# Kernel optimization log

Measured on AMD Instinct MI355X. Metric: run time of the kernel, lower is better.

## Reference

```python
import jax, jax.numpy as jnp
import numpy as np

D_MODEL = 4096
EXPERTS = 64
TOPK = 2


def setup_inputs() -> dict:
    key = jax.random.key(0)
    kx, kw = jax.random.split(key)
    x = jax.random.normal(kx, (4, 4096, D_MODEL), dtype=jnp.float32)
    # nn.Linear(input_size, expert_num, bias=False) weight, stored as [D, E] for x @ W
    W = jax.random.normal(kw, (D_MODEL, EXPERTS), dtype=jnp.float32) * (1.0 / np.sqrt(D_MODEL))
    return {"x": x, "W": W}


def reference(x, W):
    # logits = GateL(x): [B, S, E]
    logits = jnp.einsum("bsd,de->bse", x, W)
    y = jax.nn.softmax(logits, axis=-1)
    # top-k mask: scatter ones at top-k expert slots, zero elsewhere
    _, topk_idx = jax.lax.top_k(y, TOPK)            # [B, S, k]
    mask = jnp.sum(jax.nn.one_hot(topk_idx, EXPERTS, dtype=y.dtype), axis=-2)  # [B, S, E]
    y = y * mask
    return (y, logits)
```

## Files before the change

### kernel.cpp

```cpp
#include <hip/hip_runtime.h>
#include <hip/hip_bf16.h>


typedef float f32x4 __attribute__((ext_vector_type(4)));
typedef __bf16 bf16x8 __attribute__((ext_vector_type(8)));

#define MFMA16(a, b, c) __builtin_amdgcn_mfma_f32_16x16x32_bf16((a), (b), (c), 0, 0, 0)

__global__ __launch_bounds__(256) void k_prep_w(const float* __restrict__ W,
                                                __bf16* __restrict__ wsW) {
  const int kc = blockIdx.x;
  const int t = threadIdx.x;
  const int kk0 = t >> 4;
  const int n0 = (t & 15) << 2;
  for (int i = 0; i < 2; ++i) {
    const int kk = kk0 + (i << 4);
    const float4 w4 = *(const float4*)(W + (size_t)(kc * 32 + kk) * 64 + n0);
    const float f[4] = {w4.x, w4.y, w4.z, w4.w};
    for (int j = 0; j < 4; ++j) {
      const int n = n0 + j;
      const __bf16 h = (__bf16)f[j];
      const __bf16 l = (__bf16)(f[j] - (float)h);
      const int base = (kc << 12) + ((n >> 4) << 10) + ((n & 15) << 5) + kk;
      wsW[base] = h;
      wsW[base + 512] = l;
    }
  }
}

__device__ __forceinline__ void split8(const float4 a, const float4 b,
                                       bf16x8& hi, bf16x8& lo) {
  const float f[8] = {a.x, a.y, a.z, a.w, b.x, b.y, b.z, b.w};
#pragma unroll
  for (int i = 0; i < 8; ++i) {
    const unsigned u = __builtin_bit_cast(unsigned, f[i]);
    hi[i] = __builtin_bit_cast(__bf16, (unsigned short)(u >> 16));
    lo[i] = (__bf16)(f[i] - __builtin_bit_cast(float, u & 0xFFFF0000u));
  }
}

__global__ __launch_bounds__(256, 2) void k_gate(const float* __restrict__ x,
                                                 const __bf16* __restrict__ wsW,
                                                 float* __restrict__ y,
                                                 float* __restrict__ logits) {
  const int t = threadIdx.x;
  const int w = t >> 6, l = t & 63;
  const int tb = blockIdx.x * 32;
  const int mt = w & 1, nh = w >> 1;
  const int q = l >> 4, ln = l & 15;

  const float* xp = x + (size_t)(tb + mt * 16 + ln) * 4096 + q * 8;
  const __bf16* wq = wsW + nh * 2048 + ln * 32 + q * 8;
  const __bf16* wp0 = wq;
  const __bf16* wp1 = wq + 4096;
  const __bf16* wp2 = wq + 8192;
  const __bf16* wp3 = wq + 12288;

  f32x4 acc0 = {0.f, 0.f, 0.f, 0.f};
  f32x4 acc1 = {0.f, 0.f, 0.f, 0.f};

  float4 xa[4], xb[4];
  bf16x8 wh0[4], wl0[4], wh1[4], wl1[4];

#define LOADX(S) do {                                                   \
    xa[S] = *(const float4*)(xp + (S) * 32);                            \
    xb[S] = *(const float4*)(xp + (S) * 32 + 4);                        \
  } while (0)
#define LOADW(S, P) do {                                                \
    wh0[S] = *(const bf16x8*)((P));                                     \
    wl0[S] = *(const bf16x8*)((P) + 512);                               \
    wh1[S] = *(const bf16x8*)((P) + 1024);                              \
    wl1[S] = *(const bf16x8*)((P) + 1536);                              \
  } while (0)
#define COMP(S) do {                                                    \
    bf16x8 ah, al;                                                      \
    split8(xa[S], xb[S], ah, al);                                       \
    acc0 = MFMA16(ah, wh0[S], acc0);                                    \
    acc0 = MFMA16(al, wh0[S], acc0);                                    \
    acc0 = MFMA16(ah, wl0[S], acc0);                                    \
    acc0 = MFMA16(al, wl0[S], acc0);                                    \
    acc1 = MFMA16(ah, wh1[S], acc1);                                    \
    acc1 = MFMA16(al, wh1[S], acc1);                                    \
    acc1 = MFMA16(ah, wl1[S], acc1);                                    \
    acc1 = MFMA16(al, wl1[S], acc1);                                    \
  } while (0)

  LOADX(0); LOADX(1); LOADX(2); LOADX(3);
  LOADW(0, wp0); LOADW(1, wp1); LOADW(2, wp2); LOADW(3, wp3);
  xp += 128; wp0 += 16384; wp1 += 16384; wp2 += 16384; wp3 += 16384;

  for (int it = 0; it < 31; ++it) {
    COMP(0); LOADX(0); LOADW(0, wp0);
    COMP(1); LOADX(1); LOADW(1, wp1);
    COMP(2); LOADX(2); LOADW(2, wp2);
    COMP(3); LOADX(3); LOADW(3, wp3);
    xp += 128; wp0 += 16384; wp1 += 16384; wp2 += 16384; wp3 += 16384;
  }
  COMP(0); COMP(1); COMP(2); COMP(3);
#undef LOADX
#undef LOADW
#undef COMP

  __shared__ float lt[32 * 65];
  const int col = nh * 32 + ln;
#pragma unroll
  for (int r = 0; r < 4; ++r) {
    const int row = mt * 16 + q * 4 + r;
    lt[row * 65 + col] = acc0[r];
    lt[row * 65 + col + 16] = acc1[r];
    logits[(size_t)(tb + row) * 64 + col] = acc0[r];
    logits[(size_t)(tb + row) * 64 + col + 16] = acc1[r];
  }
  __syncthreads();

#pragma unroll
  for (int i = 0; i < 8; ++i) {
    const int tok = w * 8 + i;
    const float v = lt[tok * 65 + l];
    float bv = v; int bi = l;
    for (int off = 32; off; off >>= 1) {
      const float ov = __shfl_xor(bv, off);
      const int oi = __shfl_xor(bi, off);
      if (ov > bv || (ov == bv && oi < bi)) { bv = ov; bi = oi; }
    }
    const int i1 = bi;
    const float m1 = bv;
    float cv = (l == i1) ? -3.402823466e38f : v;
    int ci = l;
    for (int off = 32; off; off >>= 1) {
      const float ov = __shfl_xor(cv, off);
      const int oi = __shfl_xor(ci, off);
      if (ov > cv || (ov == cv && oi < ci)) { cv = ov; ci = oi; }
    }
    const float e = __expf(v - m1);
    float s = e;
    for (int off = 32; off; off >>= 1) s += __shfl_xor(s, off);
    y[(size_t)(tb + tok) * 64 + l] = (l == i1 || l == ci) ? (e / s) : 0.0f;
  }
}

extern "C" void kernel_launch(void* const* d_in, const int* in_sizes, int n_in,
                              void* d_out, int out_size, void* d_ws, size_t ws_size,
                              hipStream_t stream) {
  (void)in_sizes; (void)n_in; (void)out_size; (void)ws_size;
  const float* x = (const float*)d_in[0];
  const float* W = (const float*)d_in[1];
  float* out = (float*)d_out;
  float* yout = out;
  float* logits = out + 1048576;
  __bf16* wsW = (__bf16*)d_ws;

  k_prep_w<<<128, 256, 0, stream>>>(W, wsW);
  k_gate<<<512, 256, 0, stream>>>(x, wsW, yout, logits);
}
```

Before: 404.5 us.

## Stream x and W tiles through LDS with async global_load_lds pipeline

```diff
diff --git a/kernel.cpp b/kernel.cpp
--- a/kernel.cpp
+++ b/kernel.cpp
@@ -7,28 +7,32 @@
 
 #define MFMA16(a, b, c) __builtin_amdgcn_mfma_f32_16x16x32_bf16((a), (b), (c), 0, 0, 0)
 
+__device__ __forceinline__ void gload_lds16(const void* g, void* l) {
+  __builtin_amdgcn_global_load_lds((const __attribute__((address_space(1))) void*)g,
+                                   (__attribute__((address_space(3))) void*)l, 16, 0, 0);
+}
+
 __global__ __launch_bounds__(256) void k_prep_w(const float* __restrict__ W,
                                                 __bf16* __restrict__ wsW) {
-  const int kc = blockIdx.x;
+  const int c = blockIdx.x;
   const int t = threadIdx.x;
-  const int kk0 = t >> 4;
-  const int n0 = (t & 15) << 2;
-  for (int i = 0; i < 2; ++i) {
-    const int kk = kk0 + (i << 4);
-    const float4 w4 = *(const float4*)(W + (size_t)(kc * 32 + kk) * 64 + n0);
-    const float f[4] = {w4.x, w4.y, w4.z, w4.w};
-    for (int j = 0; j < 4; ++j) {
-      const int n = n0 + j;
-      const __bf16 h = (__bf16)f[j];
-      const __bf16 l = (__bf16)(f[j] - (float)h);
-      const int base = (kc << 12) + ((n >> 4) << 10) + ((n & 15) << 5) + kk;
-      wsW[base] = h;
-      wsW[base + 512] = l;
-    }
+  const int e = t & 63;
+  const int q = t >> 6;
+  const int nh = e >> 5, ntl = (e >> 4) & 1, ln = e & 15;
+  bf16x8 hi8, lo8;
+#pragma unroll
+  for (int j = 0; j < 8; ++j) {
+    const float w = W[(size_t)(c * 32 + q * 8 + j) * 64 + e];
+    const __bf16 h = (__bf16)w;
+    hi8[j] = h;
+    lo8[j] = (__bf16)(w - (float)h);
   }
+  __bf16* base = wsW + (size_t)c * 4096 + nh * 2048 + ntl * 1024 + q * 128 + ln * 8;
+  *(bf16x8*)base = hi8;
+  *(bf16x8*)(base + 512) = lo8;
 }
 
-__device__ __forceinline__ void split8(const float4 a, const float4 b,
+__device__ __forceinline__ void split8(const f32x4 a, const f32x4 b,
                                        bf16x8& hi, bf16x8& lo) {
   const float f[8] = {a.x, a.y, a.z, a.w, b.x, b.y, b.z, b.w};
 #pragma unroll
@@ -43,65 +47,79 @@
                                                  const __bf16* __restrict__ wsW,
                                                  float* __restrict__ y,
                                                  float* __restrict__ logits) {
-  const int t = threadIdx.x;
-  const int w = t >> 6, l = t & 63;
+  __shared__ __align__(16) char smem[57344];
+  const int t = threadIdx.x, w = t >> 6, l = t & 63;
   const int tb = blockIdx.x * 32;
   const int mt = w & 1, nh = w >> 1;
   const int q = l >> 4, ln = l & 15;
 
-  const float* xp = x + (size_t)(tb + mt * 16 + ln) * 4096 + q * 8;
-  const __bf16* wq = wsW + nh * 2048 + ln * 32 + q * 8;
-  const __bf16* wp0 = wq;
-  const __bf16* wp1 = wq + 4096;
-  const __bf16* wp2 = wq + 8192;
-  const __bf16* wp3 = wq + 12288;
+  char* xw = smem + w * 6144;
+  char* ww = smem + 24576 + w * 8192;
+
+  const int r0 = l >> 3, g0 = (l & 7) ^ (r0 & 7);
+  const int r1 = 8 + (l >> 3), g1 = (l & 7) ^ (r1 & 7);
+  const float* xp0 = x + (size_t)(tb + mt * 16 + r0) * 4096 + g0 * 4;
+  const float* xp1 = x + (size_t)(tb + mt * 16 + r1) * 4096 + g1 * 4;
+  const __bf16* wg = wsW + nh * 2048 + l * 8;
+
+  const int rA = ln;
+  const int offA0 = (rA * 8 + ((2 * q) ^ (rA & 7))) * 16;
+  const int offA1 = (rA * 8 + ((2 * q + 1) ^ (rA & 7))) * 16;
+  const int offW = q * 256 + ln * 16;
+
+  auto stageX = [&](int st, int c) {
+    char* d = xw + st * 2048 + l * 16;
+    gload_lds16(xp0 + (size_t)c * 32, d);
+    gload_lds16(xp1 + (size_t)c * 32, d + 1024);
+  };
+  auto stageW = [&](int st, int c) {
+    char* d = ww + st * 4096 + l * 16;
+    const __bf16* s = wg + (size_t)c * 4096;
+    gload_lds16(s, d);
+    gload_lds16(s + 512, d + 1024);
+    gload_lds16(s + 1024, d + 2048);
+    gload_lds16(s + 1536, d + 3072);
+  };
 
   f32x4 acc0 = {0.f, 0.f, 0.f, 0.f};
   f32x4 acc1 = {0.f, 0.f, 0.f, 0.f};
 
-  float4 xa[4], xb[4];
-  bf16x8 wh0[4], wl0[4], wh1[4], wl1[4];
+  stageX(0, 0); stageW(0, 0); stageX(1, 1); stageW(1, 1); stageX(2, 2);
 
-#define LOADX(S) do {                                                   \
-    xa[S] = *(const float4*)(xp + (S) * 32);                            \
-    xb[S] = *(const float4*)(xp + (S) * 32 + 4);                        \
-  } while (0)
-#define LOADW(S, P) do {                                                \
-    wh0[S] = *(const bf16x8*)((P));                                     \
-    wl0[S] = *(const bf16x8*)((P) + 512);                               \
-    wh1[S] = *(const bf16x8*)((P) + 1024);                              \
-    wl1[S] = *(const bf16x8*)((P) + 1536);                              \
-  } while (0)
-#define COMP(S) do {                                                    \
-    bf16x8 ah, al;                                                      \
-    split8(xa[S], xb[S], ah, al);                                       \
-    acc0 = MFMA16(ah, wh0[S], acc0);                                    \
-    acc0 = MFMA16(al, wh0[S], acc0);                                    \
-    acc0 = MFMA16(ah, wl0[S], acc0);                                    \
-    acc0 = MFMA16(al, wl0[S], acc0);                                    \
-    acc1 = MFMA16(ah, wh1[S], acc1);                                    \
-    acc1 = MFMA16(al, wh1[S], acc1);                                    \
-    acc1 = MFMA16(ah, wl1[S], acc1);                                    \
-    acc1 = MFMA16(al, wl1[S], acc1);                                    \
-  } while (0)
+  int st = 0, stw = 0;
+  for (int c = 0; c < 128; ++c) {
+    if (c < 126)       asm volatile("s_waitcnt vmcnt(8)" ::: "memory");
+    else if (c == 126) asm volatile("s_waitcnt vmcnt(6)" ::: "memory");
+    else               asm volatile("s_waitcnt vmcnt(0)" ::: "memory");
 
-  LOADX(0); LOADX(1); LOADX(2); LOADX(3);
-  LOADW(0, wp0); LOADW(1, wp1); LOADW(2, wp2); LOADW(3, wp3);
-  xp += 128; wp0 += 16384; wp1 += 16384; wp2 += 16384; wp3 += 16384;
+    const char* xb = xw + st * 2048;
+    const char* wb = ww + stw * 4096;
+    const f32x4 A = *(const f32x4*)(xb + offA0);
+    const f32x4 B = *(const f32x4*)(xb + offA1);
+    const bf16x8 wh0 = *(const bf16x8*)(wb + offW);
+    const bf16x8 wl0 = *(const bf16x8*)(wb + offW + 1024);
+    const bf16x8 wh1 = *(const bf16x8*)(wb + offW + 2048);
+    const bf16x8 wl1 = *(const bf16x8*)(wb + offW + 3072);
 
-  for (int it = 0; it < 31; ++it) {
-    COMP(0); LOADX(0); LOADW(0, wp0);
-    COMP(1); LOADX(1); LOADW(1, wp1);
-    COMP(2); LOADX(2); LOADW(2, wp2);
-    COMP(3); LOADX(3); LOADW(3, wp3);
-    xp += 128; wp0 += 16384; wp1 += 16384; wp2 += 16384; wp3 += 16384;
+    bf16x8 ah, al;
+    split8(A, B, ah, al);
+    acc0 = MFMA16(ah, wh0, acc0);
+    acc0 = MFMA16(al, wh0, acc0);
+    acc0 = MFMA16(ah, wl0, acc0);
+    acc0 = MFMA16(al, wl0, acc0);
+    acc1 = MFMA16(ah, wh1, acc1);
+    acc1 = MFMA16(al, wh1, acc1);
+    acc1 = MFMA16(ah, wl1, acc1);
+    acc1 = MFMA16(al, wl1, acc1);
+
+    if (c < 126) stageW(stw, c + 2);
+    if (c < 125) stageX(st, c + 3);
+    st = (st == 2) ? 0 : st + 1;
+    stw ^= 1;
   }
-  COMP(0); COMP(1); COMP(2); COMP(3);
-#undef LOADX
-#undef LOADW
-#undef COMP
 
-  __shared__ float lt[32 * 65];
+  __syncthreads();
+  float* lt = (float*)smem;
   const int col = nh * 32 + ln;
 #pragma unroll
   for (int r = 0; r < 4; ++r) {
```

After: 415.7 us. 1.03x slower.
